# Kernel tuning notes

Hardware: AMD Instinct MI355X
Metric: run time of the kernel (lower is better)

## Reference

```python
import jax, jax.numpy as jnp
import numpy as np

ALPHA = 0.2  # LeakyReLU negative slope
NEG_INF = -9e15


def gat_layer(h_in, adj_mask, W, a, concat):
    """Classic pyGAT dense GraphAttentionLayer (eval mode, dropout=identity).
    h_in: [B, N, Fin], adj_mask: [N, N] bool, W: [Fin, Fout], a: [2*Fout, 1].
    """
    h = jnp.einsum('bnf,fo->bno', h_in, W)          # [B, N, Fout]
    Fo = W.shape[1]
    f1 = h @ a[:Fo, 0]                               # [B, N] scores for source
    f2 = h @ a[Fo:, 0]                               # [B, N] scores for target
    e = jax.nn.leaky_relu(f1[:, :, None] + f2[:, None, :], negative_slope=ALPHA)
    e = jnp.where(adj_mask[None, :, :], e, NEG_INF)  # mask non-edges
    attn = jax.nn.softmax(e, axis=-1)                # normalize over neighbors
    out = jnp.einsum('bij,bjo->bio', attn, h)        # weighted aggregation
    return jax.nn.elu(out) if concat else out


def setup_inputs() -> dict:
    key = jax.random.key(0)
    ks = jax.random.split(key, 7)
    B, T, N = 2, 17, 1024
    nfeat, nhid, nclass, nheads = 64, 64, 64, 4
    x = jax.random.normal(ks[0], (B, T, N, nfeat), dtype=jnp.float32)
    adj = jax.random.randint(ks[1], (N, N), 0, 2, dtype=jnp.int32)
    W_heads = jax.random.normal(ks[2], (nheads, nfeat, nhid), dtype=jnp.float32) / np.sqrt(nfeat)
    a_heads = jax.random.normal(ks[3], (nheads, 2 * nhid, 1), dtype=jnp.float32) / np.sqrt(2 * nhid)
    W_out = jax.random.normal(ks[4], (nhid * nheads, nclass), dtype=jnp.float32) / np.sqrt(nhid * nheads)
    a_out = jax.random.normal(ks[5], (2 * nclass, 1), dtype=jnp.float32) / np.sqrt(2 * nclass)
    return {"x": x, "adj": adj, "W_heads": W_heads, "a_heads": a_heads,
            "W_out": W_out, "a_out": a_out, "pred_step": 1}


def reference(x, adj, W_heads, a_heads, W_out, a_out, pred_step):
    B, T, N, F = x.shape
    Tp = T - pred_step
    mask = adj > 0
    # All time steps are independent -> fold (B, Tp) into one batch axis.
    xt = x[:, :Tp].reshape(B * Tp, N, F)
    nheads = W_heads.shape[0]
    heads = [gat_layer(xt, mask, W_heads[h], a_heads[h], concat=True)
             for h in range(nheads)]
    hcat = jnp.concatenate(heads, axis=-1)           # [B*Tp, N, nhid*nheads]
    out = jax.nn.relu(gat_layer(hcat, mask, W_out, a_out, concat=False))
    return out.reshape(B, Tp, N, -1)
```

## Files before the change

### kernel.cpp

```cpp
#include <hip/hip_runtime.h>
#include <hip/hip_bf16.h>

typedef short bf16x8 __attribute__((ext_vector_type(8)));
typedef float f32x4 __attribute__((ext_vector_type(4)));
typedef _Float16 half8 __attribute__((ext_vector_type(8)));
typedef _Float16 half4 __attribute__((ext_vector_type(4)));
typedef __fp16 cvt2_t __attribute__((ext_vector_type(2)));

#define N_NODES 1024
#define FDIM 64
#define NG 32
#define LOG2E 1.44269504088896f

__global__ __launch_bounds__(256) void k_prep(const int* __restrict__ adj,
                                              const float* __restrict__ Wh,
                                              const float* __restrict__ Wo,
                                              __hip_bfloat16* __restrict__ Madd,
                                              _Float16* __restrict__ wt1,
                                              _Float16* __restrict__ wt2) {
    const int bb = blockIdx.x, t = threadIdx.x;
    if (bb < 128) {
        int w = bb * 256 + t;
        const int* p = adj + (size_t)w * 32;
        union { bf16x8 v[4]; __hip_bfloat16 hh[32]; } u;
#pragma unroll
        for (int b = 0; b < 32; b++)
            u.hh[b] = __float2bfloat16(p[b] > 0 ? 0.f : -2048.f);
        bf16x8* dst = (bf16x8*)(Madd + (size_t)w * 32);
#pragma unroll
        for (int q = 0; q < 4; q++) dst[q] = u.v[q];
    } else if (bb < 132) {
        const int row = (bb - 128) * 64 + (t >> 2);
        const int kq = t & 3;
        const float* src = Wh + (size_t)(row >> 6) * 4096 + (row & 63);
#pragma unroll
        for (int kk = 0; kk < 16; kk += 8) {
            const int k0 = kq * 16 + kk;
            union { half8 v; cvt2_t c[4]; } pk_;
#pragma unroll
            for (int j = 0; j < 8; j += 2)
                pk_.c[j >> 1] = __builtin_amdgcn_cvt_pkrtz(src[(k0 + j) * 64],
                                                           src[(k0 + j + 1) * 64]);
            *(half8*)(wt1 + (size_t)row * 64 + k0) = pk_.v;
        }
    } else {
        const int o = (bb - 132) * 16 + (t >> 4);
        const int k0 = (t & 15) * 16;
        const float* src = Wo + o;
#pragma unroll
        for (int kk = 0; kk < 16; kk += 8) {
            union { half8 v; cvt2_t c[4]; } pk_;
#pragma unroll
            for (int j = 0; j < 8; j += 2)
                pk_.c[j >> 1] = __builtin_amdgcn_cvt_pkrtz(src[(k0 + kk + j) * 64],
                                                           src[(k0 + kk + j + 1) * 64]);
            *(half8*)(wt2 + (size_t)o * 256 + k0 + kk) = pk_.v;
        }
    }
}

__global__ __launch_bounds__(512, 2) void k_proj1(const float* __restrict__ x,
                                                  const _Float16* __restrict__ wt1,
                                                  const float* __restrict__ ah,
                                                  _Float16* __restrict__ H1T,
                                                  float* __restrict__ F1,
                                                  float* __restrict__ F2) {
    __shared__ _Float16 xs[128][64];
    const int t = threadIdx.x;
    const int nb = blockIdx.x, g = blockIdx.y;
    const int n0 = nb * 128;
    const int b = g >> 4, tstep = g & 15;

    {
        const int r = t >> 2, cq = t & 3;
        const float* xr = x + (((size_t)(b * 17 + tstep) * N_NODES + n0 + r) * FDIM) + cq * 16;
        float4 v0 = *(const float4*)(xr);
        float4 v1 = *(const float4*)(xr + 4);
        float4 v2 = *(const float4*)(xr + 8);
        float4 v3 = *(const float4*)(xr + 12);
        union { half8 v; cvt2_t c[4]; } u0, u1;
        u0.c[0] = __builtin_amdgcn_cvt_pkrtz(v0.x, v0.y);
        u0.c[1] = __builtin_amdgcn_cvt_pkrtz(v0.z, v0.w);
        u0.c[2] = __builtin_amdgcn_cvt_pkrtz(v1.x, v1.y);
        u0.c[3] = __builtin_amdgcn_cvt_pkrtz(v1.z, v1.w);
        u1.c[0] = __builtin_amdgcn_cvt_pkrtz(v2.x, v2.y);
        u1.c[1] = __builtin_amdgcn_cvt_pkrtz(v2.z, v2.w);
        u1.c[2] = __builtin_amdgcn_cvt_pkrtz(v3.x, v3.y);
        u1.c[3] = __builtin_amdgcn_cvt_pkrtz(v3.z, v3.w);
        *(half8*)&xs[r][((2 * cq) ^ (r & 7)) * 8] = u0.v;
        *(half8*)&xs[r][((2 * cq + 1) ^ (r & 7)) * 8] = u1.v;
    }
    __syncthreads();

    const int wv = t >> 6, ln = t & 63, li = ln & 15, grp = ln >> 4;
    const int arow = wv * 16 + li;

    f32x4 acc[16];
#pragma unroll
    for (int q = 0; q < 16; q++) acc[q] = (f32x4){0.f, 0.f, 0.f, 0.f};

#pragma unroll
    for (int s = 0; s < 2; s++) {
        half8 af = *(const half8*)&xs[arow][((s * 4 + grp) ^ (arow & 7)) * 8];
#pragma unroll
        for (int tile = 0; tile < 16; tile++) {
            half8 bf = *(const half8*)(wt1 + (size_t)(tile * 16 + li) * 64 + s * 32 + grp * 8);
            acc[tile] = __builtin_amdgcn_mfma_f32_16x16x32_f16(af, bf, acc[tile], 0, 0, 0);
        }
    }

    const int nbase = n0 + wv * 16 + grp * 4;
#pragma unroll
    for (int h = 0; h < 4; h++) {
        float p1[4] = {0.f, 0.f, 0.f, 0.f}, p2[4] = {0.f, 0.f, 0.f, 0.f};
#pragma unroll
        for (int ot = 0; ot < 4; ot++) {
            float a1v = ah[h * 128 + ot * 16 + li];
            float a2v = ah[h * 128 + 64 + ot * 16 + li];
            f32x4 A = acc[h * 4 + ot];
#pragma unroll
            for (int r = 0; r < 4; r++) {
                p1[r] = fmaf(A[r], a1v, p1[r]);
                p2[r] = fmaf(A[r], a2v, p2[r]);
            }
        }
#pragma unroll
        for (int m = 1; m < 16; m <<= 1)
#pragma unroll
            for (int r = 0; r < 4; r++) {
                p1[r] += __shfl_xor(p1[r], m);
                p2[r] += __shfl_xor(p2[r], m);
            }
        if (li == 0) {
            const size_t gh = (size_t)h * NG + g;
#pragma unroll
            for (int r = 0; r < 4; r++) {
                F1[gh * N_NODES + nbase + r] = p1[r] * LOG2E;
                F2[gh * N_NODES + nbase + r] = p2[r] * LOG2E;
            }
        }
    }
#pragma unroll
    for (int tile = 0; tile < 16; tile++) {
        const int h = tile >> 2, ot = tile & 3;
        union { half4 v; cvt2_t c[2]; } st;
        st.c[0] = __builtin_amdgcn_cvt_pkrtz(acc[tile][0], acc[tile][1]);
        st.c[1] = __builtin_amdgcn_cvt_pkrtz(acc[tile][2], acc[tile][3]);
        _Float16* dst = H1T + (((size_t)h * NG + g) * FDIM + ot * 16 + li) * N_NODES + nbase;
        *(half4*)dst = st.v;
    }
}

template<int CONCAT>
__global__ __launch_bounds__(512, 4) void k_attn(
    const _Float16* __restrict__ HT,
    const float* __restrict__ F1,
    const float* __restrict__ F2,
    const __hip_bfloat16* __restrict__ Madd,
    _Float16* __restrict__ HC,
    float* __restrict__ out)
{
    __shared__ _Float16 vt[2][64][256];
    __shared__ float f2s[N_NODES];
    const int t = threadIdx.x;
    const int g = blockIdx.x, h = blockIdx.y, nb = blockIdx.z;
    const int i0 = nb * 128;
    const size_t gidx = CONCAT ? ((size_t)h * NG + g) : (size_t)g;

    ((float2*)f2s)[t] = ((const float2*)(F2 + gidx * N_NODES))[t];

    const int wv = t >> 6, ln = t & 63;
    const int li = ln & 15, grp = ln >> 4, jb = grp * 8;
    const int lx = li & 7;
    const int il = wv * 16 + li;
    const float f1v = F1[gidx * N_NODES + i0 + il];

    const _Float16* Hg = HT + gidx * (size_t)(FDIM * N_NODES);
    const int srow = wv * 8 + (ln >> 3);
    const int swu = (ln & 7) ^ (srow & 7);
    const _Float16* srcb = Hg + (size_t)srow * N_NODES + (ln & 7) * 8;
    const __hip_bfloat16* Mp = Madd + (size_t)(i0 + il) * N_NODES + jb;

    f32x4 acc[4], acc5;
#pragma unroll
    for (int q = 0; q < 4; q++) acc[q] = (f32x4){0.f, 0.f, 0.f, 0.f};
    acc5 = (f32x4){0.f, 0.f, 0.f, 0.f};

    union { half8 v; unsigned short s[8]; } onesu;
#pragma unroll
    for (int q = 0; q < 8; q++) onesu.s[q] = 0x3C00;
    const half8 ones = onesu.v;

    half8 stg[4];
#pragma unroll
    for (int k2 = 0; k2 < 4; k2++) stg[k2] = *(const half8*)(srcb + k2 * 64);
#pragma unroll
    for (int k2 = 0; k2 < 4; k2++)
        *(half8*)&vt[0][srow][(k2 * 8 + swu) * 8] = stg[k2];
#pragma unroll
    for (int k2 = 0; k2 < 4; k2++) stg[k2] = *(const half8*)(srcb + 256 + k2 * 64);
    bf16x8 m0 = *(const bf16x8*)Mp;
    bf16x8 m1 = *(const bf16x8*)(Mp + 32);
    __syncthreads();

    for (int jt = 0; jt < 4; jt++) {
        if (jt < 3) {
#pragma unroll
            for (int k2 = 0; k2 < 4; k2++)
                *(half8*)&vt[(jt + 1) & 1][srow][(k2 * 8 + swu) * 8] = stg[k2];
        }
        if (jt < 2) {
#pragma unroll
            for (int k2 = 0; k2 < 4; k2++)
                stg[k2] = *(const half8*)(srcb + (jt + 2) * 256 + k2 * 64);
        }

#pragma unroll
        for (int jc = 0; jc < 8; jc++) {
            union { bf16x8 v; unsigned u[4]; } mc;
            mc.v = m0;
            m0 = m1;
            if (!(jt == 3 && jc >= 6))
                m1 = *(const bf16x8*)(Mp + 64);
            Mp += 32;

            const float* f2p = &f2s[jt * 256 + jc * 32 + jb];
            float4 fa = *(const float4*)f2p;
            float4 fb = *(const float4*)(f2p + 4);
            union { half8 v; cvt2_t c[4]; } afr;
            {
                float mlo, mhi, s0, s1;
                mlo = __uint_as_float(mc.u[0] << 16);
                mhi = __uint_as_float(mc.u[0] & 0xffff0000u);
                s0 = f1v + fa.x + mlo; s1 = f1v + fa.y + mhi;
                s0 = fmaxf(s0, 0.2f * s0); s1 = fmaxf(s1, 0.2f * s1);
                afr.c[0] = __builtin_amdgcn_cvt_pkrtz(__builtin_amdgcn_exp2f(s0),
                                                      __builtin_amdgcn_exp2f(s1));
                mlo = __uint_as_float(mc.u[1] << 16);
                mhi = __uint_as_float(mc.u[1] & 0xffff0000u);
                s0 = f1v + fa.z + mlo; s1 = f1v + fa.w + mhi;
                s0 = fmaxf(s0, 0.2f * s0); s1 = fmaxf(s1, 0.2f * s1);
                afr.c[1] = __builtin_amdgcn_cvt_pkrtz(__builtin_amdgcn_exp2f(s0),
                                                      __builtin_amdgcn_exp2f(s1));
                mlo = __uint_as_float(mc.u[2] << 16);
                mhi = __uint_as_float(mc.u[2] & 0xffff0000u);
                s0 = f1v + fb.x + mlo; s1 = f1v + fb.y + mhi;
                s0 = fmaxf(s0, 0.2f * s0); s1 = fmaxf(s1, 0.2f * s1);
                afr.c[2] = __builtin_amdgcn_cvt_pkrtz(__builtin_amdgcn_exp2f(s0),
                                                      __builtin_amdgcn_exp2f(s1));
                mlo = __uint_as_float(mc.u[3] << 16);
                mhi = __uint_as_float(mc.u[3] & 0xffff0000u);
                s0 = f1v + fb.z + mlo; s1 = f1v + fb.w + mhi;
                s0 = fmaxf(s0, 0.2f * s0); s1 = fmaxf(s1, 0.2f * s1);
                afr.c[3] = __builtin_amdgcn_cvt_pkrtz(__builtin_amdgcn_exp2f(s0),
                                                      __builtin_amdgcn_exp2f(s1));
            }
            const int ub = (jc >> 1) * 8 + (((jc & 1) * 4 + grp) ^ lx);
#pragma unroll
            for (int q = 0; q < 4; q++) {
                half8 bfr = *(const half8*)&vt[jt & 1][q * 16 + li][ub * 8];
                acc[q] = __builtin_amdgcn_mfma_f32_16x16x32_f16(afr.v, bfr, acc[q], 0, 0, 0);
            }
            acc5 = __builtin_amdgcn_mfma_f32_16x16x32_f16(afr.v, ones, acc5, 0, 0, 0);
        }
        if (jt < 3) __syncthreads();
    }

    float rin[4];
#pragma unroll
    for (int r2 = 0; r2 < 4; r2++) rin[r2] = 1.0f / acc5[r2];

    if (CONCAT) {
        _Float16* HCg = HC + (size_t)g * N_NODES * 256 + h * 64;
#pragma unroll
        for (int q = 0; q < 4; q++)
#pragma unroll
            for (int r2 = 0; r2 < 4; r2++) {
                int irow = wv * 16 + grp * 4 + r2;
                float v = acc[q][r2] * rin[r2];
                v = v > 0.f ? v : expm1f(v);
                HCg[(size_t)(i0 + irow) * 256 + q * 16 + li] = (_Float16)v;
            }
    } else {
        float* og = out + (size_t)g * N_NODES * FDIM;
#pragma unroll
        for (int q = 0; q < 4; q++)
#pragma unroll
            for (int r2 = 0; r2 < 4; r2++) {
                int irow = wv * 16 + grp * 4 + r2;
                float v = acc[q][r2] * rin[r2];
                og[(size_t)(i0 + irow) * FDIM + q * 16 + li] = v > 0.f ? v : 0.f;
            }
    }
}

__global__ __launch_bounds__(512, 2) void k_proj2(const _Float16* __restrict__ HC,
                                                  const _Float16* __restrict__ wt2,
                                                  const float* __restrict__ ao,
                                                  _Float16* __restrict__ H2T,
                                                  float* __restrict__ F1b,
                                                  float* __restrict__ F2b) {
    __shared__ _Float16 xs[128][256];
    const int t = threadIdx.x;
    const int nb = blockIdx.x, g = blockIdx.y;
    const int n0 = nb * 128;

    {
        const int r = t >> 2, cq = t & 3;
        const _Float16* src = HC + ((size_t)g * N_NODES + n0 + r) * 256 + cq * 64;
#pragma unroll
        for (int uu = 0; uu < 8; uu++) {
            int u = cq * 8 + uu;
            half8 v = *(const half8*)(src + uu * 8);
            int us = (u & 24) | ((u ^ r) & 7);
            *(half8*)&xs[r][us * 8] = v;
        }
    }
    __syncthreads();

    const int wv = t >> 6, ln = t & 63, li = ln & 15, grp = ln >> 4;
    const int arow = wv * 16 + li;

    f32x4 acc[4];
#pragma unroll
    for (int q = 0; q < 4; q++) acc[q] = (f32x4){0.f, 0.f, 0.f, 0.f};

#pragma unroll
    for (int s = 0; s < 8; s++) {
        int u = s * 4 + grp;
        int us = (u & 24) | ((u ^ arow) & 7);
        half8 af = *(const half8*)&xs[arow][us * 8];
#pragma unroll
        for (int tile = 0; tile < 4; tile++) {
            half8 bf = *(const half8*)(wt2 + (size_t)(tile * 16 + li) * 256 + s * 32 + grp * 8);
            acc[tile] = __builtin_amdgcn_mfma_f32_16x16x32_f16(af, bf, acc[tile], 0, 0, 0);
        }
    }

    const int nbase = n0 + wv * 16 + grp * 4;
    {
        float p1[4] = {0.f, 0.f, 0.f, 0.f}, p2[4] = {0.f, 0.f, 0.f, 0.f};
#pragma unroll
        for (int ot = 0; ot < 4; ot++) {
            float a1v = ao[ot * 16 + li];
            float a2v = ao[64 + ot * 16 + li];
            f32x4 A = acc[ot];
#pragma unroll
            for (int r = 0; r < 4; r++) {
                p1[r] = fmaf(A[r], a1v, p1[r]);
                p2[r] = fmaf(A[r], a2v, p2[r]);
            }
        }
#pragma unroll
        for (int m = 1; m < 16; m <<= 1)
#pragma unroll
            for (int r = 0; r < 4; r++) {
                p1[r] += __shfl_xor(p1[r], m);
                p2[r] += __shfl_xor(p2[r], m);
            }
        if (li == 0) {
#pragma unroll
            for (int r = 0; r < 4; r++) {
                F1b[(size_t)g * N_NODES + nbase + r] = p1[r] * LOG2E;
                F2b[(size_t)g * N_NODES + nbase + r] = p2[r] * LOG2E;
            }
        }
    }
#pragma unroll
    for (int tile = 0; tile < 4; tile++) {
        union { half4 v; cvt2_t c[2]; } st;
        st.c[0] = __builtin_amdgcn_cvt_pkrtz(acc[tile][0], acc[tile][1]);
        st.c[1] = __builtin_amdgcn_cvt_pkrtz(acc[tile][2], acc[tile][3]);
        _Float16* dst = H2T + ((size_t)g * FDIM + tile * 16 + li) * N_NODES + nbase;
        *(half4*)dst = st.v;
    }
}

extern "C" void kernel_launch(void* const* d_in, const int* in_sizes, int n_in,
                              void* d_out, int out_size, void* d_ws, size_t ws_size,
                              hipStream_t stream) {
    const float* x  = (const float*)d_in[0];
    const int* adj  = (const int*)d_in[1];
    const float* Wh = (const float*)d_in[2];
    const float* ah = (const float*)d_in[3];
    const float* Wo = (const float*)d_in[4];
    const float* ao = (const float*)d_in[5];

    char* ws = (char*)d_ws;
    __hip_bfloat16* Madd = (__hip_bfloat16*)(ws);
    _Float16* wt1 = (_Float16*)(ws + 2097152);
    _Float16* wt2 = (_Float16*)(ws + 2129920);
    float* F1  = (float*)(ws + 2162688);
    float* F2  = (float*)(ws + 2686976);
    float* F1b = (float*)(ws + 3211264);
    float* F2b = (float*)(ws + 3342336);
    _Float16* H1T = (_Float16*)(ws + 3473408);
    _Float16* HC  = (_Float16*)(ws + 3473408 + 16777216);
    _Float16* H2T = (_Float16*)(ws + 3473408 + 33554432);
    float* out = (float*)d_out;

    k_prep   <<<dim3(136),       dim3(256), 0, stream>>>(adj, Wh, Wo, Madd, wt1, wt2);
    k_proj1  <<<dim3(8, 32),     dim3(512), 0, stream>>>(x, wt1, ah, H1T, F1, F2);
    k_attn<1><<<dim3(32, 4, 8),  dim3(512), 0, stream>>>(H1T, F1, F2, Madd, HC, nullptr);
    k_proj2  <<<dim3(8, 32),     dim3(512), 0, stream>>>(HC, wt2, ao, H2T, F1b, F2b);
    k_attn<0><<<dim3(32, 1, 8),  dim3(512), 0, stream>>>(H2T, F1b, F2b, Madd, nullptr, out);
}
```

Baseline: 111.3 us.

## Store adjacency mask as bytes and apply it multiplicatively after exp

Replaces the bf16 additive mask (0 / -2048) with a one-byte 0/1 mask, halving the mask bytes the attention kernels read. The mask is applied by multiplying exp2(score) by the byte value instead of adding a large negative before exp. Mask loads are prefetched per 256-column tile into a register double buffer, and the F2 shared-memory reads are software-pipelined one step ahead. Register pressure goes up, and masking after exp changes behaviour if any row ever has no neighbours.

```diff
diff --git a/kernel.cpp b/kernel.cpp
--- a/kernel.cpp
+++ b/kernel.cpp
@@ -15,20 +15,23 @@
 __global__ __launch_bounds__(256) void k_prep(const int* __restrict__ adj,
                                               const float* __restrict__ Wh,
                                               const float* __restrict__ Wo,
-                                              __hip_bfloat16* __restrict__ Madd,
+                                              unsigned char* __restrict__ Mbyte,
                                               _Float16* __restrict__ wt1,
                                               _Float16* __restrict__ wt2) {
     const int bb = blockIdx.x, t = threadIdx.x;
     if (bb < 128) {
         int w = bb * 256 + t;
         const int* p = adj + (size_t)w * 32;
-        union { bf16x8 v[4]; __hip_bfloat16 hh[32]; } u;
-#pragma unroll
-        for (int b = 0; b < 32; b++)
-            u.hh[b] = __float2bfloat16(p[b] > 0 ? 0.f : -2048.f);
-        bf16x8* dst = (bf16x8*)(Madd + (size_t)w * 32);
-#pragma unroll
-        for (int q = 0; q < 4; q++) dst[q] = u.v[q];
+        unsigned r[8];
+#pragma unroll
+        for (int q = 0; q < 8; q++) {
+            int4 a = ((const int4*)p)[q];
+            r[q] = (a.x > 0 ? 1u : 0u) | (a.y > 0 ? 1u << 8 : 0u) |
+                   (a.z > 0 ? 1u << 16 : 0u) | (a.w > 0 ? 1u << 24 : 0u);
+        }
+        uint4* dst = (uint4*)(Mbyte + (size_t)w * 32);
+        dst[0] = (uint4){r[0], r[1], r[2], r[3]};
+        dst[1] = (uint4){r[4], r[5], r[6], r[7]};
     } else if (bb < 132) {
         const int row = (bb - 128) * 64 + (t >> 2);
         const int kq = t & 3;
@@ -156,7 +159,7 @@
     const _Float16* __restrict__ HT,
     const float* __restrict__ F1,
     const float* __restrict__ F2,
-    const __hip_bfloat16* __restrict__ Madd,
+    const unsigned char* __restrict__ Mb,
     _Float16* __restrict__ HC,
     float* __restrict__ out)
 {
@@ -179,7 +182,7 @@
     const int srow = wv * 8 + (ln >> 3);
     const int swu = (ln & 7) ^ (srow & 7);
     const _Float16* srcb = Hg + (size_t)srow * N_NODES + (ln & 7) * 8;
-    const __hip_bfloat16* Mp = Madd + (size_t)(i0 + il) * N_NODES + jb;
+    const unsigned char* Mrow = Mb + (size_t)(i0 + il) * N_NODES + jb;
 
     f32x4 acc[4], acc5;
 #pragma unroll
@@ -192,6 +195,7 @@
     const half8 ones = onesu.v;
 
     half8 stg[4];
+    uint2 mbuf[2][8];
 #pragma unroll
     for (int k2 = 0; k2 < 4; k2++) stg[k2] = *(const half8*)(srcb + k2 * 64);
 #pragma unroll
@@ -199,15 +203,23 @@
         *(half8*)&vt[0][srow][(k2 * 8 + swu) * 8] = stg[k2];
 #pragma unroll
     for (int k2 = 0; k2 < 4; k2++) stg[k2] = *(const half8*)(srcb + 256 + k2 * 64);
-    bf16x8 m0 = *(const bf16x8*)Mp;
-    bf16x8 m1 = *(const bf16x8*)(Mp + 32);
+#pragma unroll
+    for (int q = 0; q < 8; q++) mbuf[0][q] = *(const uint2*)(Mrow + q * 32);
     __syncthreads();
 
+    const float* f2p = &f2s[jb];
+    float4 fa = *(const float4*)f2p;
+    float4 fb = *(const float4*)(f2p + 4);
+
+#pragma unroll
     for (int jt = 0; jt < 4; jt++) {
         if (jt < 3) {
 #pragma unroll
             for (int k2 = 0; k2 < 4; k2++)
                 *(half8*)&vt[(jt + 1) & 1][srow][(k2 * 8 + swu) * 8] = stg[k2];
+#pragma unroll
+            for (int q = 0; q < 8; q++)
+                mbuf[(jt + 1) & 1][q] = *(const uint2*)(Mrow + (jt + 1) * 256 + q * 32);
         }
         if (jt < 2) {
 #pragma unroll
@@ -217,44 +229,46 @@
 
 #pragma unroll
         for (int jc = 0; jc < 8; jc++) {
-            union { bf16x8 v; unsigned u[4]; } mc;
-            mc.v = m0;
-            m0 = m1;
-            if (!(jt == 3 && jc >= 6))
-                m1 = *(const bf16x8*)(Mp + 64);
-            Mp += 32;
-
-            const float* f2p = &f2s[jt * 256 + jc * 32 + jb];
-            float4 fa = *(const float4*)f2p;
-            float4 fb = *(const float4*)(f2p + 4);
+            const uint2 w = mbuf[jt & 1][jc];
+            const float4 cfa = fa, cfb = fb;
+            if (!(jt == 3 && jc == 7)) {
+                fa = *(const float4*)(f2p + 32);
+                fb = *(const float4*)(f2p + 36);
+            }
+            f2p += 32;
+
+            float b0 = (float)(unsigned char)(w.x);
+            float b1 = (float)(unsigned char)(w.x >> 8);
+            float b2 = (float)(unsigned char)(w.x >> 16);
+            float b3 = (float)(w.x >> 24);
+            float b4 = (float)(unsigned char)(w.y);
+            float b5 = (float)(unsigned char)(w.y >> 8);
+            float b6 = (float)(unsigned char)(w.y >> 16);
+            float b7 = (float)(w.y >> 24);
+
             union { half8 v; cvt2_t c[4]; } afr;
-            {
-                float mlo, mhi, s0, s1;
-                mlo = __uint_as_float(mc.u[0] << 16);
-                mhi = __uint_as_float(mc.u[0] & 0xffff0000u);
-                s0 = f1v + fa.x + mlo; s1 = f1v + fa.y + mhi;
-                s0 = fmaxf(s0, 0.2f * s0); s1 = fmaxf(s1, 0.2f * s1);
-                afr.c[0] = __builtin_amdgcn_cvt_pkrtz(__builtin_amdgcn_exp2f(s0),
-                                                      __builtin_amdgcn_exp2f(s1));
-                mlo = __uint_as_float(mc.u[1] << 16);
-                mhi = __uint_as_float(mc.u[1] & 0xffff0000u);
-                s0 = f1v + fa.z + mlo; s1 = f1v + fa.w + mhi;
-                s0 = fmaxf(s0, 0.2f * s0); s1 = fmaxf(s1, 0.2f * s1);
-                afr.c[1] = __builtin_amdgcn_cvt_pkrtz(__builtin_amdgcn_exp2f(s0),
-                                                      __builtin_amdgcn_exp2f(s1));
-                mlo = __uint_as_float(mc.u[2] << 16);
-                mhi = __uint_as_float(mc.u[2] & 0xffff0000u);
-                s0 = f1v + fb.x + mlo; s1 = f1v + fb.y + mhi;
-                s0 = fmaxf(s0, 0.2f * s0); s1 = fmaxf(s1, 0.2f * s1);
-                afr.c[2] = __builtin_amdgcn_cvt_pkrtz(__builtin_amdgcn_exp2f(s0),
-                                                      __builtin_amdgcn_exp2f(s1));
-                mlo = __uint_as_float(mc.u[3] << 16);
-                mhi = __uint_as_float(mc.u[3] & 0xffff0000u);
-                s0 = f1v + fb.z + mlo; s1 = f1v + fb.w + mhi;
-                s0 = fmaxf(s0, 0.2f * s0); s1 = fmaxf(s1, 0.2f * s1);
-                afr.c[3] = __builtin_amdgcn_cvt_pkrtz(__builtin_amdgcn_exp2f(s0),
-                                                      __builtin_amdgcn_exp2f(s1));
-            }
+            float s0, s1, p0, p1;
+            s0 = f1v + cfa.x; s1 = f1v + cfa.y;
+            s0 = fmaxf(s0, 0.2f * s0); s1 = fmaxf(s1, 0.2f * s1);
+            p0 = __builtin_amdgcn_exp2f(s0) * b0;
+            p1 = __builtin_amdgcn_exp2f(s1) * b1;
+            afr.c[0] = __builtin_amdgcn_cvt_pkrtz(p0, p1);
+            s0 = f1v + cfa.z; s1 = f1v + cfa.w;
+            s0 = fmaxf(s0, 0.2f * s0); s1 = fmaxf(s1, 0.2f * s1);
+            p0 = __builtin_amdgcn_exp2f(s0) * b2;
+            p1 = __builtin_amdgcn_exp2f(s1) * b3;
+            afr.c[1] = __builtin_amdgcn_cvt_pkrtz(p0, p1);
+            s0 = f1v + cfb.x; s1 = f1v + cfb.y;
+            s0 = fmaxf(s0, 0.2f * s0); s1 = fmaxf(s1, 0.2f * s1);
+            p0 = __builtin_amdgcn_exp2f(s0) * b4;
+            p1 = __builtin_amdgcn_exp2f(s1) * b5;
+            afr.c[2] = __builtin_amdgcn_cvt_pkrtz(p0, p1);
+            s0 = f1v + cfb.z; s1 = f1v + cfb.w;
+            s0 = fmaxf(s0, 0.2f * s0); s1 = fmaxf(s1, 0.2f * s1);
+            p0 = __builtin_amdgcn_exp2f(s0) * b6;
+            p1 = __builtin_amdgcn_exp2f(s1) * b7;
+            afr.c[3] = __builtin_amdgcn_cvt_pkrtz(p0, p1);
+
             const int ub = (jc >> 1) * 8 + (((jc & 1) * 4 + grp) ^ lx);
 #pragma unroll
             for (int q = 0; q < 4; q++) {
@@ -387,21 +401,21 @@
     const float* ao = (const float*)d_in[5];
 
     char* ws = (char*)d_ws;
-    __hip_bfloat16* Madd = (__hip_bfloat16*)(ws);
-    _Float16* wt1 = (_Float16*)(ws + 2097152);
-    _Float16* wt2 = (_Float16*)(ws + 2129920);
-    float* F1  = (float*)(ws + 2162688);
-    float* F2  = (float*)(ws + 2686976);
-    float* F1b = (float*)(ws + 3211264);
-    float* F2b = (float*)(ws + 3342336);
-    _Float16* H1T = (_Float16*)(ws + 3473408);
-    _Float16* HC  = (_Float16*)(ws + 3473408 + 16777216);
-    _Float16* H2T = (_Float16*)(ws + 3473408 + 33554432);
+    unsigned char* Mbyte = (unsigned char*)(ws);
+    _Float16* wt1 = (_Float16*)(ws + 1048576);
+    _Float16* wt2 = (_Float16*)(ws + 1081344);
+    float* F1  = (float*)(ws + 1114112);
+    float* F2  = (float*)(ws + 1638400);
+    float* F1b = (float*)(ws + 2162688);
+    float* F2b = (float*)(ws + 2293760);
+    _Float16* H1T = (_Float16*)(ws + 2424832);
+    _Float16* HC  = (_Float16*)(ws + 2424832 + 16777216);
+    _Float16* H2T = (_Float16*)(ws + 2424832 + 33554432);
     float* out = (float*)d_out;
 
-    k_prep   <<<dim3(136),       dim3(256), 0, stream>>>(adj, Wh, Wo, Madd, wt1, wt2);
+    k_prep   <<<dim3(136),       dim3(256), 0, stream>>>(adj, Wh, Wo, Mbyte, wt1, wt2);
     k_proj1  <<<dim3(8, 32),     dim3(512), 0, stream>>>(x, wt1, ah, H1T, F1, F2);
-    k_attn<1><<<dim3(32, 4, 8),  dim3(512), 0, stream>>>(H1T, F1, F2, Madd, HC, nullptr);
+    k_attn<1><<<dim3(32, 4, 8),  dim3(512), 0, stream>>>(H1T, F1, F2, Mbyte, HC, nullptr);
     k_proj2  <<<dim3(8, 32),     dim3(512), 0, stream>>>(HC, wt2, ao, H2T, F1b, F2b);
-    k_attn<0><<<dim3(32, 1, 8),  dim3(512), 0, stream>>>(H2T, F1b, F2b, Madd, nullptr, out);
+    k_attn<0><<<dim3(32, 1, 8),  dim3(512), 0, stream>>>(H2T, F1b, F2b, Mbyte, nullptr, out);
 }
```

Result: no change. 109.2 us (-1.9%).
